# Optimization experiments

Hardware: AMD Instinct MI355X
Metric: run time of the kernel (lower is better)

## Reference

```python
import jax, jax.numpy as jnp
import numpy as np

B, N, K, D, M, KEY_DIM = 2, 16384, 32, 128, 2, 64


def _mlp(x, w_in, b_in, w_hid, b_hid, w_out, b_out, act):
    # FCBlock: in->hidden, 3 hidden layers, hidden->out; activation on all but last.
    h = act(x @ w_in + b_in)
    for i in range(w_hid.shape[0]):
        h = act(h @ w_hid[i] + b_hid[i])
    return h @ w_out + b_out


def setup_inputs() -> dict:
    key = jax.random.key(0)
    ks = jax.random.split(key, 16)
    rn = lambda k, s, sc=1.0: jax.random.normal(k, s, dtype=jnp.float32) * sc
    w_scale = 0.05  # small init so sigmoid/affinity stay in a sane range
    return {
        'backbone_features': rn(ks[0], (B, N, D)),
        'gather_affinities': rn(ks[1], (B, M, N, K)),
        'embed_table': rn(ks[2], (M, KEY_DIM)),
        'enc_w_in': rn(ks[3], (2 * D, 128), w_scale),
        'enc_b_in': jnp.zeros((128,), jnp.float32),
        'enc_w_hid': rn(ks[4], (3, 128, 128), w_scale),
        'enc_b_hid': jnp.zeros((3, 128), jnp.float32),
        'enc_w_out': rn(ks[5], (128, KEY_DIM), w_scale),
        'enc_b_out': jnp.zeros((KEY_DIM,), jnp.float32),
        'bias_w_in': rn(ks[6], (2 * D, 128), w_scale),
        'bias_b_in': jnp.zeros((128,), jnp.float32),
        'bias_w_hid': rn(ks[7], (3, 128, 128), w_scale),
        'bias_b_hid': jnp.zeros((3, 128), jnp.float32),
        'bias_w_out': rn(ks[8], (128, 1), w_scale),
        'bias_b_out': jnp.zeros((1,), jnp.float32),
        'indices': jax.random.randint(ks[9], (3, B, N, K), 0, N),
    }


def reference(backbone_features, gather_affinities, embed_table,
              enc_w_in, enc_b_in, enc_w_hid, enc_b_hid, enc_w_out, enc_b_out,
              bias_w_in, bias_b_in, bias_w_hid, bias_b_hid, bias_w_out, bias_b_out,
              indices):
    # indices: [3, B, N, K]; channel 1 = x node ids, channel 2 = y node ids
    x_idx, y_idx = indices[1], indices[2]                       # [B, N, K]
    gather = jax.vmap(lambda feats, idx: feats[idx])            # per-batch gather
    x_feat = gather(backbone_features, x_idx)                   # [B, N, K, D]
    y_feat = gather(backbone_features, y_idx)                   # [B, N, K, D]
    edge_feat = jnp.concatenate([x_feat, y_feat], axis=-1)      # [B, N, K, 2D]

    edge_cond = _mlp(edge_feat, enc_w_in, enc_b_in, enc_w_hid, enc_b_hid,
                     enc_w_out, enc_b_out, jax.nn.relu)          # [B, N, K, KEY]
    edge_bias = _mlp(edge_feat, bias_w_in, bias_b_in, bias_w_hid, bias_b_hid,
                     bias_w_out, bias_b_out, jax.nn.gelu)[..., 0]  # [B, N, K]

    # L2 normalize (F.normalize, p=2, dim=-1, eps=1e-12)
    eps = 1e-12
    edge_cond = edge_cond / jnp.maximum(
        jnp.linalg.norm(edge_cond, axis=-1, keepdims=True), eps)
    embeds = embed_table / jnp.maximum(
        jnp.linalg.norm(embed_table, axis=-1, keepdims=True), eps)  # [M, KEY]

    attn = jax.nn.sigmoid(jnp.einsum('bnkd,md->bmnk', edge_cond, embeds))
    obj_affinity = jnp.einsum('bmnk,bmnk->bnk', attn,
                              gather_affinities - edge_bias[:, None])
    return obj_affinity
```

## Files before the change

kernel.cpp:

```cpp
#include <hip/hip_runtime.h>

typedef short frag  __attribute__((ext_vector_type(8)));
typedef float f32x4 __attribute__((ext_vector_type(4)));
typedef unsigned short u16;

#define E_TOT 1048576
#define NK    524288

#define WPK_US   174080
#define EMBN_OFF 348160
#define BB16_OFF 360448
#define WS_NEED  (BB16_OFF + 8388608)

__device__ __forceinline__ u16 f2bf(float f){
  unsigned int u = __float_as_uint(f);
  u += 0x7FFFu + ((u >> 16) & 1u);
  return (u16)(u >> 16);
}
__device__ __forceinline__ unsigned cvtpk(float lo, float hi){
  unsigned r;
  asm("v_cvt_pk_bf16_f32 %0, %1, %2" : "=v"(r) : "v"(lo), "v"(hi));
  return r;
}
__device__ __forceinline__ float frcp(float x){ return __builtin_amdgcn_rcpf(x); }
__device__ __forceinline__ float vexp2(float x){
  float r; asm("v_exp_f32 %0, %1" : "=v"(r) : "v"(x)); return r;
}
__device__ __forceinline__ float sigm(float y){
  return frcp(1.f + vexp2(-1.4426950408889634f * y));
}
__device__ __forceinline__ float gelu_f(float x){
  const float C1 = 2.0f * 0.7978845608028654f * 1.4426950408889634f;
  const float C2 = 0.044715f * C1;
  float z = x * fmaf(C2, x * x, C1);
  return x * frcp(1.f + vexp2(-z));
}

__device__ __forceinline__ void gl_lds16(const void* g, void* l){
#if __has_builtin(__builtin_amdgcn_global_load_lds)
  __builtin_amdgcn_global_load_lds(
      (const __attribute__((address_space(1))) unsigned int*)g,
      (__attribute__((address_space(3))) unsigned int*)l, 16, 0, 0);
#else
  *(uint4*)l = *(const uint4*)g;
#endif
}

template<int N> struct IC { static constexpr int value = N; };

__global__ void prep_kernel(const float* __restrict__ enc_w_in,
                            const float* __restrict__ enc_w_hid,
                            const float* __restrict__ enc_w_out,
                            const float* __restrict__ bias_w_in,
                            const float* __restrict__ bias_w_hid,
                            const float* __restrict__ bias_w_out,
                            const float* __restrict__ embed_table,
                            u16* __restrict__ wpk,
                            float* __restrict__ embn)
{
  int p = blockIdx.x * 256 + threadIdx.x;
  if (p < WPK_US) {
    const int base[12] = {0,16384,32768,49152,65536,81920,90112,106496,122880,139264,155648,172032};
    const int koff[12] = {0,128,0,0,0,0,0,128,0,0,0,0};
    const int njv[12]  = {128,128,128,128,128,64,128,128,128,128,128,1};
    const float* srcs[12] = {enc_w_in, enc_w_in, enc_w_hid, enc_w_hid+16384, enc_w_hid+32768,
                             enc_w_out, bias_w_in, bias_w_in, bias_w_hid, bias_w_hid+16384,
                             bias_w_hid+32768, bias_w_out};
    int L = 0;
    #pragma unroll
    for (int i = 1; i < 12; ++i) if (p >= base[i]) L = i;
    int r    = p - base[L];
    int f    = r >> 9;
    int lane = (r >> 3) & 63;
    int e    = r & 7;
    int s    = f & 3, t = f >> 2;
    int rho  = lane & 15, gf = lane >> 4;
    int nj   = njv[L];
    int j    = 16*t + 4*(((rho >> 2) ^ (t & 1)) & 3) + (rho & 3);
    int k    = 32*s + 8*gf + e + koff[L];
    wpk[p] = (j < nj) ? f2bf(srcs[L][k * nj + j]) : (u16)0;
  } else if (p < WPK_US + 128) {
    int q = p - WPK_US;
    int m = q >> 6;
    const float* row = embed_table + m * 64;
    float ss = 0.f;
    for (int t = 0; t < 64; ++t) { float v = row[t]; ss += v * v; }
    float nrm = fmaxf(sqrtf(ss), 1e-12f);
    embn[q] = row[q & 63] / nrm;
  }
}

__global__ void prep_backbone(const float* __restrict__ src, u16* __restrict__ dst)
{
  int i = (blockIdx.x * 256 + threadIdx.x) * 4;
  float4 v = *(const float4*)(src + i);
  unsigned lo = cvtpk(v.x, v.y), hi = cvtpk(v.z, v.w);
  *(uint2*)(dst + i) = make_uint2(lo, hi);
}

template<bool BF>
__global__ __launch_bounds__(256, 4)
void fused_kernel(const float* __restrict__ backbone,
                  const u16*   __restrict__ bb16,
                  const float* __restrict__ ga,
                  const int*   __restrict__ idx,
                  const float* __restrict__ enc_b_in,
                  const float* __restrict__ enc_b_hid,
                  const float* __restrict__ enc_b_out,
                  const float* __restrict__ bias_b_in,
                  const float* __restrict__ bias_b_hid,
                  const float* __restrict__ bias_b_out,
                  const u16*   __restrict__ wpk,
                  const float* __restrict__ embn,
                  float* __restrict__ out)
{
  __shared__ __align__(16) u16 wbuf[16384];

  const int tid  = threadIdx.x;
  const int w    = tid >> 6;
  const int lane = tid & 63;
  const int g    = lane >> 4;
  const int li   = lane & 15;
  const int eW   = blockIdx.x * 128 + w * 32;

  const int A0 = 4 * (li + 16 * ((((g & 1) << 1) | (g >> 1))));
  const int A2 = A0 ^ 64;

  auto stageW = [&](int base_us, int nfrag){
    for (int it = w; it < nfrag; it += 4)
      gl_lds16((const void*)(wpk + base_us + it * 512 + lane * 8),
               (void*)(&wbuf[it * 512]));
  };

  stageW(0, 32);

  int rxi[2], ryi[2];
  #pragma unroll
  for (int et = 0; et < 2; ++et) {
    int e  = eW + 16 * et + li;
    int b  = e >> 19;
    rxi[et] = (b << 14) + idx[E_TOT + e];
    ryi[et] = (b << 14) + idx[2 * E_TOT + e];
  }

  f32x4 acc[8][2];
  unsigned nb[2][4][4];

  union FU { unsigned u[4]; frag f; };

  auto getB_g = [&](const int* ri, int et, int s) -> frag {
    size_t off = (((size_t)(unsigned)ri[et]) << 7) + 32 * s + 8 * g;
    if constexpr (BF) {
      return *(const frag*)(bb16 + off);
    } else {
      const float* p = backbone + off;
      float4 lo = *(const float4*)p, hi = *(const float4*)(p + 4);
      FU fu;
      fu.u[0] = cvtpk(lo.x, lo.y); fu.u[1] = cvtpk(lo.z, lo.w);
      fu.u[2] = cvtpk(hi.x, hi.y); fu.u[3] = cvtpk(hi.z, hi.w);
      return fu.f;
    }
  };
  auto getBx = [&](int et, int s) -> frag { return getB_g(rxi, et, s); };
  auto getBy = [&](int et, int s) -> frag { return getB_g(ryi, et, s); };
  auto getBn = [&](int et, int s) -> frag {
    FU fu;
    fu.u[0] = nb[et][s][0]; fu.u[1] = nb[et][s][1];
    fu.u[2] = nb[et][s][2]; fu.u[3] = nb[et][s][3];
    return fu.f;
  };

  auto zeroAcc = [&](int T_){
    #pragma unroll
    for (int t = 0; t < 8; ++t)
      if (t < T_) {
        acc[t][0] = (f32x4){0.f,0.f,0.f,0.f};
        acc[t][1] = (f32x4){0.f,0.f,0.f,0.f};
      }
  };

  auto runLayer = [&](auto TC, auto getB){
    constexpr int T_ = decltype(TC)::value;
    #pragma unroll
    for (int s = 0; s < 4; ++s) {
      frag B0 = getB(0, s);
      frag B1 = getB(1, s);
      #pragma unroll
      for (int t = 0; t < T_; ++t) {
        frag A = *(const frag*)(&wbuf[(t * 4 + s) * 512 + lane * 8]);
        acc[t][0] = __builtin_amdgcn_mfma_f32_16x16x32_bf16(A, B0, acc[t][0], 0, 0, 0);
        acc[t][1] = __builtin_amdgcn_mfma_f32_16x16x32_bf16(A, B1, acc[t][1], 0, 0, 0);
      }
    }
  };

  auto finishLayer = [&](const float* bptr, bool gelu){
    #pragma unroll
    for (int sp = 0; sp < 4; ++sp) {
      unsigned pk0[2][2], pk1[2][2];
      #pragma unroll
      for (int tt = 0; tt < 2; ++tt) {
        int t = 2 * sp + tt;
        float4 bv = *(const float4*)(bptr + 16 * t + 4 * (g ^ (t & 1)));
        #pragma unroll
        for (int et = 0; et < 2; ++et) {
          float x0 = acc[t][et][0] + bv.x, x1 = acc[t][et][1] + bv.y;
          float x2 = acc[t][et][2] + bv.z, x3 = acc[t][et][3] + bv.w;
          if (gelu) { x0 = gelu_f(x0); x1 = gelu_f(x1); x2 = gelu_f(x2); x3 = gelu_f(x3); }
          else      { x0 = fmaxf(x0,0.f); x1 = fmaxf(x1,0.f); x2 = fmaxf(x2,0.f); x3 = fmaxf(x3,0.f); }
          pk0[tt][et] = cvtpk(x0, x1);
          pk1[tt][et] = cvtpk(x2, x3);
        }
      }
      #pragma unroll
      for (int et = 0; et < 2; ++et) {
        unsigned lo0 = pk0[0][et], hi0 = pk0[1][et];
        unsigned lo1 = pk1[0][et], hi1 = pk1[1][et];
        unsigned M0  = (g & 1) ? hi0 : lo0;
        unsigned M1  = (g & 1) ? hi1 : lo1;
        unsigned M0p = (g & 1) ? lo0 : hi0;
        unsigned M1p = (g & 1) ? lo1 : hi1;
        nb[et][sp][0] = (unsigned)__builtin_amdgcn_ds_bpermute(A0, (int)M0);
        nb[et][sp][1] = (unsigned)__builtin_amdgcn_ds_bpermute(A0, (int)M1);
        nb[et][sp][2] = (unsigned)__builtin_amdgcn_ds_bpermute(A2, (int)M0p);
        nb[et][sp][3] = (unsigned)__builtin_amdgcn_ds_bpermute(A2, (int)M1p);
      }
    }
  };

  zeroAcc(8);
  __syncthreads();
  runLayer(IC<8>{}, getBx);
  __syncthreads();
  stageW(16384, 32);
  __syncthreads();
  runLayer(IC<8>{}, getBy);
  __syncthreads();
  stageW(32768, 32);
  finishLayer(enc_b_in, false);
  zeroAcc(8);
  __syncthreads();
  runLayer(IC<8>{}, getBn);
  __syncthreads();
  stageW(49152, 32);
  finishLayer(enc_b_hid + 0, false);
  zeroAcc(8);
  __syncthreads();
  runLayer(IC<8>{}, getBn);
  __syncthreads();
  stageW(65536, 32);
  finishLayer(enc_b_hid + 128, false);
  zeroAcc(8);
  __syncthreads();
  runLayer(IC<8>{}, getBn);
  __syncthreads();
  stageW(81920, 16);
  finishLayer(enc_b_hid + 256, false);
  zeroAcc(4);
  __syncthreads();
  runLayer(IC<4>{}, getBn);

  __syncthreads();
  stageW(90112, 32);

  float a0v[2], a1v[2];
  {
    #pragma unroll
    for (int t = 0; t < 4; ++t) {
      float4 bv = *(const float4*)(enc_b_out + 16 * t + 4 * (g ^ (t & 1)));
      #pragma unroll
      for (int et = 0; et < 2; ++et) {
        acc[t][et][0] += bv.x; acc[t][et][1] += bv.y;
        acc[t][et][2] += bv.z; acc[t][et][3] += bv.w;
      }
    }
    #pragma unroll
    for (int et = 0; et < 2; ++et) {
      float s2 = 0.f, p0 = 0.f, p1 = 0.f;
      #pragma unroll
      for (int t = 0; t < 4; ++t) {
        float4 em0 = *(const float4*)(embn + 16 * t + 4 * (g ^ (t & 1)));
        float4 em1 = *(const float4*)(embn + 64 + 16 * t + 4 * (g ^ (t & 1)));
        #pragma unroll
        for (int r = 0; r < 4; ++r) {
          float v = acc[t][et][r];
          float e0 = (r == 0) ? em0.x : (r == 1) ? em0.y : (r == 2) ? em0.z : em0.w;
          float e1 = (r == 0) ? em1.x : (r == 1) ? em1.y : (r == 2) ? em1.z : em1.w;
          s2 = fmaf(v, v, s2);
          p0 = fmaf(v, e0, p0);
          p1 = fmaf(v, e1, p1);
        }
      }
      s2 += __shfl_xor(s2, 16); s2 += __shfl_xor(s2, 32);
      p0 += __shfl_xor(p0, 16); p0 += __shfl_xor(p0, 32);
      p1 += __shfl_xor(p1, 16); p1 += __shfl_xor(p1, 32);
      float inv = frcp(fmaxf(sqrtf(s2), 1e-12f));
      a0v[et] = sigm(p0 * inv);
      a1v[et] = sigm(p1 * inv);
    }
  }

  zeroAcc(8);
  __syncthreads();
  runLayer(IC<8>{}, getBx);
  __syncthreads();
  stageW(106496, 32);
  __syncthreads();
  runLayer(IC<8>{}, getBy);
  __syncthreads();
  stageW(122880, 32);
  finishLayer(bias_b_in, true);
  zeroAcc(8);
  __syncthreads();
  runLayer(IC<8>{}, getBn);
  __syncthreads();
  stageW(139264, 32);
  finishLayer(bias_b_hid + 0, true);
  zeroAcc(8);
  __syncthreads();
  runLayer(IC<8>{}, getBn);
  __syncthreads();
  stageW(155648, 32);
  finishLayer(bias_b_hid + 128, true);
  zeroAcc(8);
  __syncthreads();
  runLayer(IC<8>{}, getBn);
  __syncthreads();
  stageW(172032, 4);
  finishLayer(bias_b_hid + 256, true);
  zeroAcc(1);
  __syncthreads();
  runLayer(IC<1>{}, getBn);

  if (g == 0) {
    float bb0 = bias_b_out[0];
    #pragma unroll
    for (int et = 0; et < 2; ++et) {
      int e   = eW + 16 * et + li;
      int b   = e >> 19;
      int off = e & (NK - 1);
      float g0 = ga[((size_t)b << 20) + off];
      float g1 = ga[((size_t)b << 20) + NK + off];
      float bi = acc[0][et][0] + bb0;
      out[e] = a0v[et] * (g0 - bi) + a1v[et] * (g1 - bi);
    }
  }
}

extern "C" void kernel_launch(void* const* d_in, const int* in_sizes, int n_in,
                              void* d_out, int out_size, void* d_ws, size_t ws_size,
                              hipStream_t stream) {
  const float* backbone   = (const float*)d_in[0];
  const float* ga         = (const float*)d_in[1];
  const float* embed      = (const float*)d_in[2];
  const float* enc_w_in   = (const float*)d_in[3];
  const float* enc_b_in   = (const float*)d_in[4];
  const float* enc_w_hid  = (const float*)d_in[5];
  const float* enc_b_hid  = (const float*)d_in[6];
  const float* enc_w_out  = (const float*)d_in[7];
  const float* enc_b_out  = (const float*)d_in[8];
  const float* bias_w_in  = (const float*)d_in[9];
  const float* bias_b_in  = (const float*)d_in[10];
  const float* bias_w_hid = (const float*)d_in[11];
  const float* bias_b_hid = (const float*)d_in[12];
  const float* bias_w_out = (const float*)d_in[13];
  const float* bias_b_out = (const float*)d_in[14];
  const int*   indices    = (const int*)d_in[15];

  u16*   wpk  = (u16*)d_ws;
  float* embn = (float*)((char*)d_ws + EMBN_OFF);
  u16*   bb16 = (u16*)((char*)d_ws + BB16_OFF);

  hipLaunchKernelGGL(prep_kernel, dim3(681), dim3(256), 0, stream,
                     enc_w_in, enc_w_hid, enc_w_out,
                     bias_w_in, bias_w_hid, bias_w_out,
                     embed, wpk, embn);

  bool bf = (ws_size >= (size_t)WS_NEED);
  if (bf) {
    hipLaunchKernelGGL(prep_backbone, dim3(4096), dim3(256), 0, stream, backbone, bb16);
    hipLaunchKernelGGL((fused_kernel<true>), dim3(8192), dim3(256), 0, stream,
                       backbone, bb16, ga, indices,
                       enc_b_in, enc_b_hid, enc_b_out,
                       bias_b_in, bias_b_hid, bias_b_out,
                       wpk, embn, (float*)d_out);
  } else {
    hipLaunchKernelGGL((fused_kernel<false>), dim3(8192), dim3(256), 0, stream,
                       backbone, bb16, ga, indices,
                       enc_b_in, enc_b_hid, enc_b_out,
                       bias_b_in, bias_b_hid, bias_b_out,
                       wpk, embn, (float*)d_out);
  }
}
```

Before: 652.4 us.

## Read MLP weight fragments directly from global memory instead of staging through LDS

Drops the shared-memory weight buffer and the per-layer staging loads along with every block barrier. Each wave now loads its MFMA A fragments straight from the packed weight array in global memory, relying on L1/L2 caching. Accumulator zeroing is folded into the first MFMA of each layer, and launch bounds drop from 4 to 3 blocks per SM to leave more registers. The cost is that every wave issues its own global weight loads, which adds latency and cache traffic in exchange for no LDS and no synchronisation.

```diff
diff --git a/kernel.cpp b/kernel.cpp
--- a/kernel.cpp
+++ b/kernel.cpp
@@ -34,16 +34,6 @@
   const float C2 = 0.044715f * C1;
   float z = x * fmaf(C2, x * x, C1);
   return x * frcp(1.f + vexp2(-z));
-}
-
-__device__ __forceinline__ void gl_lds16(const void* g, void* l){
-#if __has_builtin(__builtin_amdgcn_global_load_lds)
-  __builtin_amdgcn_global_load_lds(
-      (const __attribute__((address_space(1))) unsigned int*)g,
-      (__attribute__((address_space(3))) unsigned int*)l, 16, 0, 0);
-#else
-  *(uint4*)l = *(const uint4*)g;
-#endif
 }
 
 template<int N> struct IC { static constexpr int value = N; };
@@ -99,7 +89,7 @@
 }
 
 template<bool BF>
-__global__ __launch_bounds__(256, 4)
+__global__ __launch_bounds__(256, 3)
 void fused_kernel(const float* __restrict__ backbone,
                   const u16*   __restrict__ bb16,
                   const float* __restrict__ ga,
@@ -114,8 +104,6 @@
                   const float* __restrict__ embn,
                   float* __restrict__ out)
 {
-  __shared__ __align__(16) u16 wbuf[16384];
-
   const int tid  = threadIdx.x;
   const int w    = tid >> 6;
   const int lane = tid & 63;
@@ -125,14 +113,6 @@
 
   const int A0 = 4 * (li + 16 * ((((g & 1) << 1) | (g >> 1))));
   const int A2 = A0 ^ 64;
-
-  auto stageW = [&](int base_us, int nfrag){
-    for (int it = w; it < nfrag; it += 4)
-      gl_lds16((const void*)(wpk + base_us + it * 512 + lane * 8),
-               (void*)(&wbuf[it * 512]));
-  };
-
-  stageW(0, 32);
 
   int rxi[2], ryi[2];
   #pragma unroll
@@ -145,6 +125,7 @@
 
   f32x4 acc[8][2];
   unsigned nb[2][4][4];
+  const f32x4 kZ = {0.f, 0.f, 0.f, 0.f};
 
   union FU { unsigned u[4]; frag f; };
 
@@ -170,26 +151,23 @@
     return fu.f;
   };
 
-  auto zeroAcc = [&](int T_){
-    #pragma unroll
-    for (int t = 0; t < 8; ++t)
-      if (t < T_) {
-        acc[t][0] = (f32x4){0.f,0.f,0.f,0.f};
-        acc[t][1] = (f32x4){0.f,0.f,0.f,0.f};
-      }
-  };
-
-  auto runLayer = [&](auto TC, auto getB){
+  auto runLayer = [&](auto TC, auto ZFC, const u16* __restrict__ wp, auto getB){
     constexpr int T_ = decltype(TC)::value;
+    constexpr bool ZF = (decltype(ZFC)::value != 0);
     #pragma unroll
     for (int s = 0; s < 4; ++s) {
       frag B0 = getB(0, s);
       frag B1 = getB(1, s);
       #pragma unroll
       for (int t = 0; t < T_; ++t) {
-        frag A = *(const frag*)(&wbuf[(t * 4 + s) * 512 + lane * 8]);
-        acc[t][0] = __builtin_amdgcn_mfma_f32_16x16x32_bf16(A, B0, acc[t][0], 0, 0, 0);
-        acc[t][1] = __builtin_amdgcn_mfma_f32_16x16x32_bf16(A, B1, acc[t][1], 0, 0, 0);
+        frag A = *(const frag*)(wp + (t * 4 + s) * 512 + lane * 8);
+        if (ZF && s == 0) {
+          acc[t][0] = __builtin_amdgcn_mfma_f32_16x16x32_bf16(A, B0, kZ, 0, 0, 0);
+          acc[t][1] = __builtin_amdgcn_mfma_f32_16x16x32_bf16(A, B1, kZ, 0, 0, 0);
+        } else {
+          acc[t][0] = __builtin_amdgcn_mfma_f32_16x16x32_bf16(A, B0, acc[t][0], 0, 0, 0);
+          acc[t][1] = __builtin_amdgcn_mfma_f32_16x16x32_bf16(A, B1, acc[t][1], 0, 0, 0);
+        }
       }
     }
   };
@@ -228,40 +206,16 @@
     }
   };
 
-  zeroAcc(8);
-  __syncthreads();
-  runLayer(IC<8>{}, getBx);
-  __syncthreads();
-  stageW(16384, 32);
-  __syncthreads();
-  runLayer(IC<8>{}, getBy);
-  __syncthreads();
-  stageW(32768, 32);
+  runLayer(IC<8>{}, IC<1>{}, wpk + 0,      getBx);
+  runLayer(IC<8>{}, IC<0>{}, wpk + 16384,  getBy);
   finishLayer(enc_b_in, false);
-  zeroAcc(8);
-  __syncthreads();
-  runLayer(IC<8>{}, getBn);
-  __syncthreads();
-  stageW(49152, 32);
+  runLayer(IC<8>{}, IC<1>{}, wpk + 32768,  getBn);
   finishLayer(enc_b_hid + 0, false);
-  zeroAcc(8);
-  __syncthreads();
-  runLayer(IC<8>{}, getBn);
-  __syncthreads();
-  stageW(65536, 32);
+  runLayer(IC<8>{}, IC<1>{}, wpk + 49152,  getBn);
   finishLayer(enc_b_hid + 128, false);
-  zeroAcc(8);
-  __syncthreads();
-  runLayer(IC<8>{}, getBn);
-  __syncthreads();
-  stageW(81920, 16);
+  runLayer(IC<8>{}, IC<1>{}, wpk + 65536,  getBn);
   finishLayer(enc_b_hid + 256, false);
-  zeroAcc(4);
-  __syncthreads();
-  runLayer(IC<4>{}, getBn);
-
-  __syncthreads();
-  stageW(90112, 32);
+  runLayer(IC<4>{}, IC<1>{}, wpk + 81920,  getBn);
 
   float a0v[2], a1v[2];
   {
@@ -300,37 +254,16 @@
     }
   }
 
-  zeroAcc(8);
-  __syncthreads();
-  runLayer(IC<8>{}, getBx);
-  __syncthreads();
-  stageW(106496, 32);
-  __syncthreads();
-  runLayer(IC<8>{}, getBy);
-  __syncthreads();
-  stageW(122880, 32);
+  runLayer(IC<8>{}, IC<1>{}, wpk + 90112,  getBx);
+  runLayer(IC<8>{}, IC<0>{}, wpk + 106496, getBy);
   finishLayer(bias_b_in, true);
-  zeroAcc(8);
-  __syncthreads();
-  runLayer(IC<8>{}, getBn);
-  __syncthreads();
-  stageW(139264, 32);
+  runLayer(IC<8>{}, IC<1>{}, wpk + 122880, getBn);
   finishLayer(bias_b_hid + 0, true);
-  zeroAcc(8);
-  __syncthreads();
-  runLayer(IC<8>{}, getBn);
-  __syncthreads();
-  stageW(155648, 32);
+  runLayer(IC<8>{}, IC<1>{}, wpk + 139264, getBn);
   finishLayer(bias_b_hid + 128, true);
-  zeroAcc(8);
-  __syncthreads();
-  runLayer(IC<8>{}, getBn);
-  __syncthreads();
-  stageW(172032, 4);
+  runLayer(IC<8>{}, IC<1>{}, wpk + 155648, getBn);
   finishLayer(bias_b_hid + 256, true);
-  zeroAcc(1);
-  __syncthreads();
-  runLayer(IC<1>{}, getBn);
+  runLayer(IC<1>{}, IC<1>{}, wpk + 172032, getBn);
 
   if (g == 0) {
     float bb0 = bias_b_out[0];
```

Result: slower. 1.144 ms (+75.4%).

## Switch MLP matmuls to 32x32x16 MFMA with permlane-swap activation relayout

Applied to the files above, without the earlier changes.

Each wave's 32-edge MLP tiles now go through mfma_f32_32x32x16_bf16 instead of pairs of 16x16x32 MFMAs. The weight packing in the prep kernel is rewritten to match, and the last bias layer is padded to 32 columns, which shifts the workspace offsets. Between layers, activations are reshuffled with v_permlane32_swap instead of four ds_bpermute calls per fragment, and accumulators are zero-seeded by the first MFMA rather than cleared separately. The goal is fewer MFMA issues and fewer LDS weight reads and cross-lane ops; in exchange, the larger 16-wide accumulators need more registers, so launch bounds drop to 3 waves per SIMD.

```diff
diff --git a/kernel.cpp b/kernel.cpp
--- a/kernel.cpp
+++ b/kernel.cpp
@@ -1,15 +1,16 @@
 #include <hip/hip_runtime.h>
 
-typedef short frag  __attribute__((ext_vector_type(8)));
-typedef float f32x4 __attribute__((ext_vector_type(4)));
+typedef short frag   __attribute__((ext_vector_type(8)));
+typedef float f32x4  __attribute__((ext_vector_type(4)));
+typedef float f32x16 __attribute__((ext_vector_type(16)));
 typedef unsigned short u16;
 
 #define E_TOT 1048576
 #define NK    524288
 
-#define WPK_US   174080
-#define EMBN_OFF 348160
-#define BB16_OFF 360448
+#define WPK_US   176128
+#define EMBN_OFF 352256
+#define BB16_OFF 352768
 #define WS_NEED  (BB16_OFF + 8388608)
 
 __device__ __forceinline__ u16 f2bf(float f){
@@ -21,6 +22,9 @@
   unsigned r;
   asm("v_cvt_pk_bf16_f32 %0, %1, %2" : "=v"(r) : "v"(lo), "v"(hi));
   return r;
+}
+__device__ __forceinline__ void plswap(unsigned &a, unsigned &b){
+  asm("v_permlane32_swap_b32 %0, %1" : "+v"(a), "+v"(b));
 }
 __device__ __forceinline__ float frcp(float x){ return __builtin_amdgcn_rcpf(x); }
 __device__ __forceinline__ float vexp2(float x){
@@ -71,13 +75,12 @@
     for (int i = 1; i < 12; ++i) if (p >= base[i]) L = i;
     int r    = p - base[L];
     int f    = r >> 9;
-    int lane = (r >> 3) & 63;
-    int e    = r & 7;
-    int s    = f & 3, t = f >> 2;
-    int rho  = lane & 15, gf = lane >> 4;
+    int q    = r & 511;
+    int lane = q >> 3, e = q & 7;
+    int t    = f >> 3, s = f & 7;
     int nj   = njv[L];
-    int j    = 16*t + 4*(((rho >> 2) ^ (t & 1)) & 3) + (rho & 3);
-    int k    = 32*s + 8*gf + e + koff[L];
+    int j    = 32*t + (lane & 31);
+    int k    = 16*s + 8*(lane >> 5) + e + koff[L];
     wpk[p] = (j < nj) ? f2bf(srcs[L][k * nj + j]) : (u16)0;
   } else if (p < WPK_US + 128) {
     int q = p - WPK_US;
@@ -99,7 +102,7 @@
 }
 
 template<bool BF>
-__global__ __launch_bounds__(256, 4)
+__global__ __launch_bounds__(256, 3)
 void fused_kernel(const float* __restrict__ backbone,
                   const u16*   __restrict__ bb16,
                   const float* __restrict__ ga,
@@ -119,12 +122,10 @@
   const int tid  = threadIdx.x;
   const int w    = tid >> 6;
   const int lane = tid & 63;
-  const int g    = lane >> 4;
-  const int li   = lane & 15;
+  const int h    = lane >> 5;
+  const int col  = lane & 31;
   const int eW   = blockIdx.x * 128 + w * 32;
-
-  const int A0 = 4 * (li + 16 * ((((g & 1) << 1) | (g >> 1))));
-  const int A2 = A0 ^ 64;
+  const int e    = eW + col;
 
   auto stageW = [&](int base_us, int nfrag){
     for (int it = w; it < nfrag; it += 4)
@@ -134,22 +135,18 @@
 
   stageW(0, 32);
 
-  int rxi[2], ryi[2];
-  #pragma unroll
-  for (int et = 0; et < 2; ++et) {
-    int e  = eW + 16 * et + li;
-    int b  = e >> 19;
-    rxi[et] = (b << 14) + idx[E_TOT + e];
-    ryi[et] = (b << 14) + idx[2 * E_TOT + e];
-  }
-
-  f32x4 acc[8][2];
-  unsigned nb[2][4][4];
+  int b = e >> 19;
+  int rxi = (b << 14) + idx[E_TOT + e];
+  int ryi = (b << 14) + idx[2 * E_TOT + e];
+
+  f32x16 acc[4];
+  unsigned nb[8][4];
+  const f32x16 kZ = {0.f,0.f,0.f,0.f, 0.f,0.f,0.f,0.f, 0.f,0.f,0.f,0.f, 0.f,0.f,0.f,0.f};
 
   union FU { unsigned u[4]; frag f; };
 
-  auto getB_g = [&](const int* ri, int et, int s) -> frag {
-    size_t off = (((size_t)(unsigned)ri[et]) << 7) + 32 * s + 8 * g;
+  auto getB_g = [&](int ri, int s) -> frag {
+    size_t off = (((size_t)(unsigned)ri) << 7) + 16 * s + 8 * h;
     if constexpr (BF) {
       return *(const frag*)(bb16 + off);
     } else {
@@ -161,189 +158,144 @@
       return fu.f;
     }
   };
-  auto getBx = [&](int et, int s) -> frag { return getB_g(rxi, et, s); };
-  auto getBy = [&](int et, int s) -> frag { return getB_g(ryi, et, s); };
-  auto getBn = [&](int et, int s) -> frag {
+  auto getBx = [&](int s) -> frag { return getB_g(rxi, s); };
+  auto getBy = [&](int s) -> frag { return getB_g(ryi, s); };
+  auto getBn = [&](int s) -> frag {
     FU fu;
-    fu.u[0] = nb[et][s][0]; fu.u[1] = nb[et][s][1];
-    fu.u[2] = nb[et][s][2]; fu.u[3] = nb[et][s][3];
+    fu.u[0] = nb[s][0]; fu.u[1] = nb[s][1];
+    fu.u[2] = nb[s][2]; fu.u[3] = nb[s][3];
     return fu.f;
   };
 
-  auto zeroAcc = [&](int T_){
+  auto runLayer = [&](auto SC, auto TC, auto ZFC, auto getB){
+    constexpr int S_ = decltype(SC)::value;
+    constexpr int T_ = decltype(TC)::value;
+    constexpr bool ZF = (decltype(ZFC)::value != 0);
     #pragma unroll
-    for (int t = 0; t < 8; ++t)
-      if (t < T_) {
-        acc[t][0] = (f32x4){0.f,0.f,0.f,0.f};
-        acc[t][1] = (f32x4){0.f,0.f,0.f,0.f};
-      }
-  };
-
-  auto runLayer = [&](auto TC, auto getB){
-    constexpr int T_ = decltype(TC)::value;
-    #pragma unroll
-    for (int s = 0; s < 4; ++s) {
-      frag B0 = getB(0, s);
-      frag B1 = getB(1, s);
+    for (int s = 0; s < S_; ++s) {
+      frag B = getB(s);
       #pragma unroll
       for (int t = 0; t < T_; ++t) {
-        frag A = *(const frag*)(&wbuf[(t * 4 + s) * 512 + lane * 8]);
-        acc[t][0] = __builtin_amdgcn_mfma_f32_16x16x32_bf16(A, B0, acc[t][0], 0, 0, 0);
-        acc[t][1] = __builtin_amdgcn_mfma_f32_16x16x32_bf16(A, B1, acc[t][1], 0, 0, 0);
+        frag A = *(const frag*)(&wbuf[(t * S_ + s) * 512 + lane * 8]);
+        if (ZF && s == 0)
+          acc[t] = __builtin_amdgcn_mfma_f32_32x32x16_bf16(A, B, kZ, 0, 0, 0);
+        else
+          acc[t] = __builtin_amdgcn_mfma_f32_32x32x16_bf16(A, B, acc[t], 0, 0, 0);
       }
     }
   };
 
   auto finishLayer = [&](const float* bptr, bool gelu){
     #pragma unroll
-    for (int sp = 0; sp < 4; ++sp) {
-      unsigned pk0[2][2], pk1[2][2];
-      #pragma unroll
-      for (int tt = 0; tt < 2; ++tt) {
-        int t = 2 * sp + tt;
-        float4 bv = *(const float4*)(bptr + 16 * t + 4 * (g ^ (t & 1)));
+    for (int t = 0; t < 4; ++t) {
+      float x[16];
+      #pragma unroll
+      for (int q = 0; q < 4; ++q) {
+        f32x4 bv = *(const f32x4*)(bptr + 32*t + 8*q + 4*h);
         #pragma unroll
-        for (int et = 0; et < 2; ++et) {
-          float x0 = acc[t][et][0] + bv.x, x1 = acc[t][et][1] + bv.y;
-          float x2 = acc[t][et][2] + bv.z, x3 = acc[t][et][3] + bv.w;
-          if (gelu) { x0 = gelu_f(x0); x1 = gelu_f(x1); x2 = gelu_f(x2); x3 = gelu_f(x3); }
-          else      { x0 = fmaxf(x0,0.f); x1 = fmaxf(x1,0.f); x2 = fmaxf(x2,0.f); x3 = fmaxf(x3,0.f); }
-          pk0[tt][et] = cvtpk(x0, x1);
-          pk1[tt][et] = cvtpk(x2, x3);
+        for (int i = 0; i < 4; ++i) x[4*q+i] = acc[t][4*q+i] + bv[i];
+      }
+      #pragma unroll
+      for (int i = 0; i < 16; ++i)
+        x[i] = gelu ? gelu_f(x[i]) : fmaxf(x[i], 0.f);
+      unsigned wv[8];
+      #pragma unroll
+      for (int i = 0; i < 8; ++i) wv[i] = cvtpk(x[2*i], x[2*i+1]);
+      plswap(wv[0], wv[2]); plswap(wv[1], wv[3]);
+      plswap(wv[4], wv[6]); plswap(wv[5], wv[7]);
+      nb[2*t][0] = wv[0]; nb[2*t][1] = wv[1]; nb[2*t][2] = wv[2]; nb[2*t][3] = wv[3];
+      nb[2*t+1][0] = wv[4]; nb[2*t+1][1] = wv[5]; nb[2*t+1][2] = wv[6]; nb[2*t+1][3] = wv[7];
+    }
+  };
+
+  __syncthreads();
+  runLayer(IC<8>{}, IC<4>{}, IC<1>{}, getBx);
+  __syncthreads();
+  stageW(16384, 32);
+  __syncthreads();
+  runLayer(IC<8>{}, IC<4>{}, IC<0>{}, getBy);
+  __syncthreads();
+  stageW(32768, 32);
+  finishLayer(enc_b_in, false);
+  __syncthreads();
+  runLayer(IC<8>{}, IC<4>{}, IC<1>{}, getBn);
+  __syncthreads();
+  stageW(49152, 32);
+  finishLayer(enc_b_hid + 0, false);
+  __syncthreads();
+  runLayer(IC<8>{}, IC<4>{}, IC<1>{}, getBn);
+  __syncthreads();
+  stageW(65536, 32);
+  finishLayer(enc_b_hid + 128, false);
+  __syncthreads();
+  runLayer(IC<8>{}, IC<4>{}, IC<1>{}, getBn);
+  __syncthreads();
+  stageW(81920, 16);
+  finishLayer(enc_b_hid + 256, false);
+  __syncthreads();
+  runLayer(IC<8>{}, IC<2>{}, IC<1>{}, getBn);
+  __syncthreads();
+  stageW(90112, 32);
+
+  float a0v, a1v;
+  {
+    float s2 = 0.f, p0 = 0.f, p1 = 0.f;
+    #pragma unroll
+    for (int t = 0; t < 2; ++t)
+      #pragma unroll
+      for (int q = 0; q < 4; ++q) {
+        f32x4 bv = *(const f32x4*)(enc_b_out + 32*t + 8*q + 4*h);
+        f32x4 e0 = *(const f32x4*)(embn + 32*t + 8*q + 4*h);
+        f32x4 e1 = *(const f32x4*)(embn + 64 + 32*t + 8*q + 4*h);
+        #pragma unroll
+        for (int i = 0; i < 4; ++i) {
+          float v = acc[t][4*q+i] + bv[i];
+          s2 = fmaf(v, v, s2);
+          p0 = fmaf(v, e0[i], p0);
+          p1 = fmaf(v, e1[i], p1);
         }
       }
-      #pragma unroll
-      for (int et = 0; et < 2; ++et) {
-        unsigned lo0 = pk0[0][et], hi0 = pk0[1][et];
-        unsigned lo1 = pk1[0][et], hi1 = pk1[1][et];
-        unsigned M0  = (g & 1) ? hi0 : lo0;
-        unsigned M1  = (g & 1) ? hi1 : lo1;
-        unsigned M0p = (g & 1) ? lo0 : hi0;
-        unsigned M1p = (g & 1) ? lo1 : hi1;
-        nb[et][sp][0] = (unsigned)__builtin_amdgcn_ds_bpermute(A0, (int)M0);
-        nb[et][sp][1] = (unsigned)__builtin_amdgcn_ds_bpermute(A0, (int)M1);
-        nb[et][sp][2] = (unsigned)__builtin_amdgcn_ds_bpermute(A2, (int)M0p);
-        nb[et][sp][3] = (unsigned)__builtin_amdgcn_ds_bpermute(A2, (int)M1p);
-      }
-    }
-  };
-
-  zeroAcc(8);
-  __syncthreads();
-  runLayer(IC<8>{}, getBx);
-  __syncthreads();
-  stageW(16384, 32);
-  __syncthreads();
-  runLayer(IC<8>{}, getBy);
-  __syncthreads();
-  stageW(32768, 32);
-  finishLayer(enc_b_in, false);
-  zeroAcc(8);
-  __syncthreads();
-  runLayer(IC<8>{}, getBn);
-  __syncthreads();
-  stageW(49152, 32);
-  finishLayer(enc_b_hid + 0, false);
-  zeroAcc(8);
-  __syncthreads();
-  runLayer(IC<8>{}, getBn);
-  __syncthreads();
-  stageW(65536, 32);
-  finishLayer(enc_b_hid + 128, false);
-  zeroAcc(8);
-  __syncthreads();
-  runLayer(IC<8>{}, getBn);
-  __syncthreads();
-  stageW(81920, 16);
-  finishLayer(enc_b_hid + 256, false);
-  zeroAcc(4);
-  __syncthreads();
-  runLayer(IC<4>{}, getBn);
-
-  __syncthreads();
-  stageW(90112, 32);
-
-  float a0v[2], a1v[2];
-  {
-    #pragma unroll
-    for (int t = 0; t < 4; ++t) {
-      float4 bv = *(const float4*)(enc_b_out + 16 * t + 4 * (g ^ (t & 1)));
-      #pragma unroll
-      for (int et = 0; et < 2; ++et) {
-        acc[t][et][0] += bv.x; acc[t][et][1] += bv.y;
-        acc[t][et][2] += bv.z; acc[t][et][3] += bv.w;
-      }
-    }
-    #pragma unroll
-    for (int et = 0; et < 2; ++et) {
-      float s2 = 0.f, p0 = 0.f, p1 = 0.f;
-      #pragma unroll
-      for (int t = 0; t < 4; ++t) {
-        float4 em0 = *(const float4*)(embn + 16 * t + 4 * (g ^ (t & 1)));
-        float4 em1 = *(const float4*)(embn + 64 + 16 * t + 4 * (g ^ (t & 1)));
-        #pragma unroll
-        for (int r = 0; r < 4; ++r) {
-          float v = acc[t][et][r];
-          float e0 = (r == 0) ? em0.x : (r == 1) ? em0.y : (r == 2) ? em0.z : em0.w;
-          float e1 = (r == 0) ? em1.x : (r == 1) ? em1.y : (r == 2) ? em1.z : em1.w;
-          s2 = fmaf(v, v, s2);
-          p0 = fmaf(v, e0, p0);
-          p1 = fmaf(v, e1, p1);
-        }
-      }
-      s2 += __shfl_xor(s2, 16); s2 += __shfl_xor(s2, 32);
-      p0 += __shfl_xor(p0, 16); p0 += __shfl_xor(p0, 32);
-      p1 += __shfl_xor(p1, 16); p1 += __shfl_xor(p1, 32);
-      float inv = frcp(fmaxf(sqrtf(s2), 1e-12f));
-      a0v[et] = sigm(p0 * inv);
-      a1v[et] = sigm(p1 * inv);
-    }
+    s2 += __shfl_xor(s2, 32);
+    p0 += __shfl_xor(p0, 32);
+    p1 += __shfl_xor(p1, 32);
+    float inv = frcp(fmaxf(sqrtf(s2), 1e-12f));
+    a0v = sigm(p0 * inv);
+    a1v = sigm(p1 * inv);
   }
 
-  zeroAcc(8);
-  __syncthreads();
-  runLayer(IC<8>{}, getBx);
+  __syncthreads();
+  runLayer(IC<8>{}, IC<4>{}, IC<1>{}, getBx);
   __syncthreads();
   stageW(106496, 32);
   __syncthreads();
-  runLayer(IC<8>{}, getBy);
+  runLayer(IC<8>{}, IC<4>{}, IC<0>{}, getBy);
   __syncthreads();
   stageW(122880, 32);
   finishLayer(bias_b_in, true);
-  zeroAcc(8);
-  __syncthreads();
-  runLayer(IC<8>{}, getBn);
+  __syncthreads();
+  runLayer(IC<8>{}, IC<4>{}, IC<1>{}, getBn);
   __syncthreads();
   stageW(139264, 32);
   finishLayer(bias_b_hid + 0, true);
-  zeroAcc(8);
-  __syncthreads();
-  runLayer(IC<8>{}, getBn);
+  __syncthreads();
+  runLayer(IC<8>{}, IC<4>{}, IC<1>{}, getBn);
   __syncthreads();
   stageW(155648, 32);
   finishLayer(bias_b_hid + 128, true);
-  zeroAcc(8);
-  __syncthreads();
-  runLayer(IC<8>{}, getBn);
-  __syncthreads();
-  stageW(172032, 4);
+  __syncthreads();
+  runLayer(IC<8>{}, IC<4>{}, IC<1>{}, getBn);
+  __syncthreads();
+  stageW(172032, 8);
   finishLayer(bias_b_hid + 256, true);
-  zeroAcc(1);
-  __syncthreads();
-  runLayer(IC<1>{}, getBn);
-
-  if (g == 0) {
-    float bb0 = bias_b_out[0];
-    #pragma unroll
-    for (int et = 0; et < 2; ++et) {
-      int e   = eW + 16 * et + li;
-      int b   = e >> 19;
-      int off = e & (NK - 1);
-      float g0 = ga[((size_t)b << 20) + off];
-      float g1 = ga[((size_t)b << 20) + NK + off];
-      float bi = acc[0][et][0] + bb0;
-      out[e] = a0v[et] * (g0 - bi) + a1v[et] * (g1 - bi);
-    }
+  __syncthreads();
+  runLayer(IC<8>{}, IC<1>{}, IC<1>{}, getBn);
+
+  if (lane < 32) {
+    float bi = acc[0][0] + bias_b_out[0];
+    int off = e & (NK - 1);
+    float g0 = ga[((size_t)b << 20) + off];
+    float g1 = ga[((size_t)b << 20) + NK + off];
+    out[e] = a0v * (g0 - bi) + a1v * (g1 - bi);
   }
 }
 
@@ -371,7 +323,7 @@
   float* embn = (float*)((char*)d_ws + EMBN_OFF);
   u16*   bb16 = (u16*)((char*)d_ws + BB16_OFF);
 
-  hipLaunchKernelGGL(prep_kernel, dim3(681), dim3(256), 0, stream,
+  hipLaunchKernelGGL(prep_kernel, dim3(689), dim3(256), 0, stream,
                      enc_w_in, enc_w_hid, enc_w_out,
                      bias_w_in, bias_w_hid, bias_w_out,
                      embed, wpk, embn);
```

After: 612.6 us. -6.1%, faster.
